# Performance work log

Measured on AMD Instinct MI355X. Metric: run time of the kernel, lower is better.

The kernel has to match this reference:

```python
import jax, jax.numpy as jnp
import numpy as np

N = 50000      # nodes per graph (= num hyperedges, forced by the stack ops)
E = 800000     # incidence pairs per graph
L = 16         # max nodes per hyperedge (padded with index 0)
F_IN = 128     # in_channels
D1 = 256       # dim_1
D2 = D1 // 4   # conv2 out dim = FusionAttention in_size
H_ATT = 128    # FusionAttention hidden_size
EPS = 1e-15


def setup_inputs() -> dict:
    key = jax.random.key(0)
    ks = jax.random.split(key, 32)
    inp = {}
    for i in range(4):
        inp[f"x{i}"] = jax.random.normal(ks[i], (N, F_IN), jnp.float32)
        nidx = jax.random.randint(ks[4 + i], (E,), 0, N, dtype=jnp.int32)
        eidx = jax.random.randint(ks[8 + i], (E,), 0, N, dtype=jnp.int32)
        inp[f"ei{i}"] = jnp.stack([nidx, eidx])  # [2, E]
        hn = jax.random.randint(ks[12 + i], (N, L), 0, N + 1, dtype=jnp.int32)
        inp[f"hnode{i}"] = hn
        # hye_len = number of real (non-padding) entries per hyperedge
        inp[f"hlen{i}"] = jnp.sum(hn > 0, axis=1, keepdims=True).astype(jnp.float32)
    # shared Hgnn params (PyG HypergraphConv: lin without bias + separate bias)
    inp["W1"] = jax.random.normal(ks[16], (F_IN, D1), jnp.float32) / np.sqrt(F_IN).astype(np.float32)
    inp["b1"] = jnp.zeros((D1,), jnp.float32)
    inp["W2"] = jax.random.normal(ks[17], (D1, D2), jnp.float32) / np.sqrt(D1).astype(np.float32)
    inp["b2"] = jnp.zeros((D2,), jnp.float32)
    # two FusionAttention heads: Linear(D2,H_ATT)+Tanh, Linear(H_ATT,1,bias=False)
    for name, a, b in [("ac", 18, 19), ("am", 20, 21)]:
        inp[f"{name}_W1"] = jax.random.normal(ks[a], (D2, H_ATT), jnp.float32) / np.sqrt(D2).astype(np.float32)
        inp[f"{name}_b1"] = jnp.zeros((H_ATT,), jnp.float32)
        inp[f"{name}_W2"] = jax.random.normal(ks[b], (H_ATT, 1), jnp.float32) / np.sqrt(H_ATT).astype(np.float32)
    return inp


def _hconv(x, node_idx, edge_idx, W, b):
    """PyG HypergraphConv (heads=1, unit hyperedge weights):
    X' = D^-1 H B^-1 H^T (X W) + b, via two segment-sum passes."""
    x = x @ W  # [N, out]
    ones = jnp.ones(node_idx.shape, x.dtype)
    deg_n = jax.ops.segment_sum(ones, node_idx, num_segments=N)
    d_inv = jnp.where(deg_n > 0, 1.0 / deg_n, 0.0)
    deg_e = jax.ops.segment_sum(ones, edge_idx, num_segments=N)
    b_inv = jnp.where(deg_e > 0, 1.0 / deg_e, 0.0)
    # node -> hyperedge: m_e = B^-1[e] * sum_{v in e} x[v]
    efeat = b_inv[:, None] * jax.ops.segment_sum(x[node_idx], edge_idx, num_segments=N)
    # hyperedge -> node: out_v = D^-1[v] * sum_{e : v in e} m_e
    out = d_inv[:, None] * jax.ops.segment_sum(efeat[edge_idx], node_idx, num_segments=N)
    return out + b


def _hgnn(x, ei, W1, b1, W2, b2):
    x = jax.nn.relu(_hconv(x, ei[0], ei[1], W1, b1))
    return jax.nn.relu(_hconv(x, ei[0], ei[1], W2, b2))


def _hye_emb(node_emb, hlen, hnode):
    # prepend zero row so padding index 0 gathers zeros
    padded = jnp.concatenate([jnp.zeros((1, node_emb.shape[1]), node_emb.dtype), node_emb], axis=0)
    seq = padded[hnode]                    # [M, L, F]
    return jnp.sum(seq, axis=1) / (hlen + EPS)


def _fusion_attn(z, W1, b1, W2):
    # z: [N, 4, d]
    w = (jnp.tanh(z @ W1 + b1) @ W2).mean(0)      # [4, 1]
    beta = jax.nn.softmax(w, axis=0)              # [4, 1]
    return jnp.sum(beta * z, axis=1)              # [N, d]


def reference(x0, x1, x2, x3, ei0, ei1, ei2, ei3,
              hlen0, hlen1, hlen2, hlen3, hnode0, hnode1, hnode2, hnode3,
              W1, b1, W2, b2, ac_W1, ac_b1, ac_W2, am_W1, am_b1, am_W2):
    x1_cm = _hgnn(x0, ei0, W1, b1, W2, b2)
    x1_mc = _hgnn(x1, ei1, W1, b1, W2, b2)
    x1_cc = _hgnn(x2, ei2, W1, b1, W2, b2)
    x1_mm = _hgnn(x3, ei3, W1, b1, W2, b2)
    x2_cm = _hye_emb(x1_cm, hlen0, hnode0)
    x2_mc = _hye_emb(x1_mc, hlen1, hnode1)
    x2_cc = _hye_emb(x1_cc, hlen2, hnode2)
    x2_mm = _hye_emb(x1_mm, hlen3, hnode3)
    x_c = jnp.stack((x1_mc, x2_cm, x1_cc, x2_cc), axis=1)  # [N, 4, D2]
    x_m = jnp.stack((x1_cm, x2_mc, x1_mm, x2_mm), axis=1)
    h_c = _fusion_attn(x_c, ac_W1, ac_b1, ac_W2)
    h_m = _fusion_attn(x_m, am_W1, am_b1, am_W2)
    return (h_c, h_m)
```

## Files before the change

kernel.cpp:

```cpp
#include <hip/hip_runtime.h>
#include <hip/hip_bf16.h>

#define NF   128
#define DD1  256
#define DD2  64
#define HATT 128

static inline int cdiv(int a, int b) { return (a + b - 1) / b; }

__global__ __launch_bounds__(256) void count_rank(const int* __restrict__ nidx,
                                                  const int* __restrict__ eidx,
                                                  int* __restrict__ deg,
                                                  int* __restrict__ rank,
                                                  int N, int E) {
    int e = blockIdx.x * 256 + threadIdx.x;
    if (e < E) {
        const int vn = nidx[e], ve = eidx[e];
        const int rn = atomicAdd(&deg[vn], 1);
        const int re = atomicAdd(&deg[N + ve], 1);
        rank[e] = rn | (re << 16);
    }
}

__global__ __launch_bounds__(256) void scan_blocks(const int* __restrict__ in,
                                                   int* __restrict__ out,
                                                   int* __restrict__ partials, int n) {
    __shared__ int s[256];
    const int base = blockIdx.x * 1024;
    const int t = threadIdx.x;
    int v[4], sum = 0;
#pragma unroll
    for (int i = 0; i < 4; i++) {
        const int idx = base + t * 4 + i;
        v[i] = (idx < n) ? in[idx] : 0;
        sum += v[i];
    }
    s[t] = sum;
    __syncthreads();
    for (int o = 1; o < 256; o <<= 1) {
        int x = 0;
        if (t >= o) x = s[t - o];
        __syncthreads();
        if (t >= o) s[t] += x;
        __syncthreads();
    }
    if (t == 255) partials[blockIdx.x] = s[255];
    int run = (t == 0) ? 0 : s[t - 1];
#pragma unroll
    for (int i = 0; i < 4; i++) {
        const int idx = base + t * 4 + i;
        if (idx < n) out[idx] = run;
        run += v[i];
    }
}

__global__ __launch_bounds__(512) void scan_partials(int* __restrict__ partials, int P) {
    __shared__ int s[512];
    const int t = threadIdx.x;
    s[t] = (t < P) ? partials[t] : 0;
    __syncthreads();
    for (int o = 1; o < 512; o <<= 1) {
        int x = 0;
        if (t >= o) x = s[t - o];
        __syncthreads();
        if (t >= o) s[t] += x;
        __syncthreads();
    }
    if (t < P) partials[t] = (t == 0) ? 0 : s[t - 1];
}

__global__ __launch_bounds__(256) void scan_add(int* __restrict__ off,
                                                const int* __restrict__ partials,
                                                int n, int total) {
    const int idx = blockIdx.x * 256 + threadIdx.x;
    if (idx < n) off[idx] += partials[idx >> 10];
    if (idx == 0) off[n] = total;
}

__global__ __launch_bounds__(256) void build_fill(const int* __restrict__ nidx,
                                                  const int* __restrict__ eidx,
                                                  const int* __restrict__ rank,
                                                  const int* __restrict__ off,
                                                  int* __restrict__ srcidx,
                                                  int N, int E, int shardSize) {
    const int shard = blockIdx.x & 7;
    const int chunk = blockIdx.x >> 3;
    const int lo = shard * shardSize;
    const int hi = lo + shardSize;
    const int base = chunk * 1024;
#pragma unroll
    for (int i = 0; i < 4; i++) {
        const int e = base + i * 256 + threadIdx.x;
        if (e < E) {
            const int vn = nidx[e], ve = eidx[e];
            const int rk = rank[e];
            if (vn >= lo && vn < hi)
                srcidx[off[vn] + (rk & 0xffff)] = ve;
            if (ve >= lo && ve < hi)
                srcidx[off[N + ve] + (rk >> 16)] = vn;
        }
    }
}

__global__ __launch_bounds__(256) void invert_deg_int(const int* __restrict__ deg,
                                                      float* __restrict__ inv, int n) {
    int t = blockIdx.x * 256 + threadIdx.x;
    if (t < n) {
        const int v = deg[t];
        inv[t] = (v > 0) ? 1.0f / (float)v : 0.f;
    }
}

struct BuildB {
    const int* nidx[4];
    const int* eidx[4];
    int* deg;
    int* rank;
    const int* off;
    int* srcidx;
    int Nn, E, shardSize;
};

__global__ __launch_bounds__(256) void count_rank_b(BuildB a) {
    const int g = blockIdx.y;
    const int e = blockIdx.x * 256 + threadIdx.x;
    if (e < a.E) {
        const int vn = a.nidx[g][e], ve = a.eidx[g][e];
        int* dg = a.deg + (size_t)g * 2 * a.Nn;
        const int rn = atomicAdd(&dg[vn], 1);
        const int re = atomicAdd(&dg[a.Nn + ve], 1);
        a.rank[(size_t)g * a.E + e] = rn | (re << 16);
    }
}

__global__ __launch_bounds__(256) void build_fill_b(BuildB a) {
    const int g = blockIdx.y;
    const int shard = blockIdx.x & 7;
    const int chunk = blockIdx.x >> 3;
    const int lo = shard * a.shardSize;
    const int hi = lo + a.shardSize;
    const int base = chunk * 1024;
    const int* __restrict__ nidx = a.nidx[g];
    const int* __restrict__ eidx = a.eidx[g];
    const int* __restrict__ rank = a.rank + (size_t)g * a.E;
    const int* __restrict__ off  = a.off + (size_t)g * 2 * a.Nn;
#pragma unroll
    for (int i = 0; i < 4; i++) {
        const int e = base + i * 256 + threadIdx.x;
        if (e < a.E) {
            const int vn = nidx[e], ve = eidx[e];
            const int rk = rank[e];
            if (vn >= lo && vn < hi)
                a.srcidx[off[vn] + (rk & 0xffff)] = ve;
            if (ve >= lo && ve < hi)
                a.srcidx[off[a.Nn + ve] + (rk >> 16)] = vn;
        }
    }
}

__global__ __launch_bounds__(256) void gather_rows_128(const float* __restrict__ src,
                                                       const int* __restrict__ off,
                                                       const int* __restrict__ srcidx,
                                                       const float* __restrict__ scale,
                                                       float* __restrict__ dst, int Nn) {
    const int row = blockIdx.x * 16 + (threadIdx.x >> 4);
    if (row >= Nn) return;
    const int c = (threadIdx.x & 15) << 2;
    const int j0 = off[row], j1 = off[row + 1];
    float4 pa = make_float4(0.f, 0.f, 0.f, 0.f);
    float4 pb = make_float4(0.f, 0.f, 0.f, 0.f);
    float4 qa = make_float4(0.f, 0.f, 0.f, 0.f);
    float4 qb = make_float4(0.f, 0.f, 0.f, 0.f);
    int j = j0;
    for (; j + 3 < j1; j += 4) {
        const int s0 = srcidx[j + 0];
        const int s1 = srcidx[j + 1];
        const int s2 = srcidx[j + 2];
        const int s3 = srcidx[j + 3];
        const float4 v0a = *(const float4*)&src[(size_t)s0 * 128 + c];
        const float4 v0b = *(const float4*)&src[(size_t)s0 * 128 + c + 64];
        const float4 v1a = *(const float4*)&src[(size_t)s1 * 128 + c];
        const float4 v1b = *(const float4*)&src[(size_t)s1 * 128 + c + 64];
        const float4 v2a = *(const float4*)&src[(size_t)s2 * 128 + c];
        const float4 v2b = *(const float4*)&src[(size_t)s2 * 128 + c + 64];
        const float4 v3a = *(const float4*)&src[(size_t)s3 * 128 + c];
        const float4 v3b = *(const float4*)&src[(size_t)s3 * 128 + c + 64];
        pa.x += v0a.x + v1a.x; pa.y += v0a.y + v1a.y;
        pa.z += v0a.z + v1a.z; pa.w += v0a.w + v1a.w;
        qa.x += v2a.x + v3a.x; qa.y += v2a.y + v3a.y;
        qa.z += v2a.z + v3a.z; qa.w += v2a.w + v3a.w;
        pb.x += v0b.x + v1b.x; pb.y += v0b.y + v1b.y;
        pb.z += v0b.z + v1b.z; pb.w += v0b.w + v1b.w;
        qb.x += v2b.x + v3b.x; qb.y += v2b.y + v3b.y;
        qb.z += v2b.z + v3b.z; qb.w += v2b.w + v3b.w;
    }
    for (; j < j1; j++) {
        const int s0 = srcidx[j];
        const float4 va = *(const float4*)&src[(size_t)s0 * 128 + c];
        const float4 vb = *(const float4*)&src[(size_t)s0 * 128 + c + 64];
        pa.x += va.x; pa.y += va.y; pa.z += va.z; pa.w += va.w;
        pb.x += vb.x; pb.y += vb.y; pb.z += vb.z; pb.w += vb.w;
    }
    float4 aca = make_float4(pa.x + qa.x, pa.y + qa.y, pa.z + qa.z, pa.w + qa.w);
    float4 acb = make_float4(pb.x + qb.x, pb.y + qb.y, pb.z + qb.z, pb.w + qb.w);
    if (scale) {
        const float s = scale[row];
        aca.x *= s; aca.y *= s; aca.z *= s; aca.w *= s;
        acb.x *= s; acb.y *= s; acb.z *= s; acb.w *= s;
    }
    *(float4*)&dst[(size_t)row * 128 + c] = aca;
    *(float4*)&dst[(size_t)row * 128 + c + 64] = acb;
}

struct Gather128H {
    const float* src[2];
    float* dst;
    const int* off;
    const int* srcidx;
    const float* dinv;
    int gbase;
    int passBase;
    int Nn;
};

__global__ __launch_bounds__(256) void gather128_h(Gather128H a) {
    const int gr = blockIdx.x * 16 + (threadIdx.x >> 4);
    if (gr >= 2 * a.Nn) return;
    const int gl = gr / a.Nn;
    const int row = gr - gl * a.Nn;
    const float* __restrict__ src = a.src[gl];
    const int ob = (a.gbase + gl) * 2 * a.Nn + a.passBase + row;
    const int c = (threadIdx.x & 15) << 2;
    const int j0 = a.off[ob], j1 = a.off[ob + 1];
    float4 pa = make_float4(0.f, 0.f, 0.f, 0.f);
    float4 pb = make_float4(0.f, 0.f, 0.f, 0.f);
    float4 qa = make_float4(0.f, 0.f, 0.f, 0.f);
    float4 qb = make_float4(0.f, 0.f, 0.f, 0.f);
    int j = j0;
    for (; j + 3 < j1; j += 4) {
        const int s0 = a.srcidx[j + 0];
        const int s1 = a.srcidx[j + 1];
        const int s2 = a.srcidx[j + 2];
        const int s3 = a.srcidx[j + 3];
        const float4 v0a = *(const float4*)&src[(size_t)s0 * 128 + c];
        const float4 v0b = *(const float4*)&src[(size_t)s0 * 128 + c + 64];
        const float4 v1a = *(const float4*)&src[(size_t)s1 * 128 + c];
        const float4 v1b = *(const float4*)&src[(size_t)s1 * 128 + c + 64];
        const float4 v2a = *(const float4*)&src[(size_t)s2 * 128 + c];
        const float4 v2b = *(const float4*)&src[(size_t)s2 * 128 + c + 64];
        const float4 v3a = *(const float4*)&src[(size_t)s3 * 128 + c];
        const float4 v3b = *(const float4*)&src[(size_t)s3 * 128 + c + 64];
        pa.x += v0a.x + v1a.x; pa.y += v0a.y + v1a.y;
        pa.z += v0a.z + v1a.z; pa.w += v0a.w + v1a.w;
        qa.x += v2a.x + v3a.x; qa.y += v2a.y + v3a.y;
        qa.z += v2a.z + v3a.z; qa.w += v2a.w + v3a.w;
        pb.x += v0b.x + v1b.x; pb.y += v0b.y + v1b.y;
        pb.z += v0b.z + v1b.z; pb.w += v0b.w + v1b.w;
        qb.x += v2b.x + v3b.x; qb.y += v2b.y + v3b.y;
        qb.z += v2b.z + v3b.z; qb.w += v2b.w + v3b.w;
    }
    for (; j < j1; j++) {
        const int s0 = a.srcidx[j];
        const float4 va = *(const float4*)&src[(size_t)s0 * 128 + c];
        const float4 vb = *(const float4*)&src[(size_t)s0 * 128 + c + 64];
        pa.x += va.x; pa.y += va.y; pa.z += va.z; pa.w += va.w;
        pb.x += vb.x; pb.y += vb.y; pb.z += vb.z; pb.w += vb.w;
    }
    float4 aca = make_float4(pa.x + qa.x, pa.y + qa.y, pa.z + qa.z, pa.w + qa.w);
    float4 acb = make_float4(pb.x + qb.x, pb.y + qb.y, pb.z + qb.z, pb.w + qb.w);
    if (a.dinv) {
        const float s = a.dinv[ob];
        aca.x *= s; aca.y *= s; aca.z *= s; aca.w *= s;
        acb.x *= s; acb.y *= s; acb.z *= s; acb.w *= s;
    }
    *(float4*)&a.dst[(size_t)gr * 128 + c] = aca;
    *(float4*)&a.dst[(size_t)gr * 128 + c + 64] = acb;
}

__global__ __launch_bounds__(256) void gather_rows_64(const float* __restrict__ src,
                                                      const int* __restrict__ off,
                                                      const int* __restrict__ srcidx,
                                                      const float* __restrict__ scale,
                                                      const float* __restrict__ post_bias,
                                                      float* __restrict__ dst, int Nn) {
    const int row = blockIdx.x * 32 + (threadIdx.x >> 3);
    if (row >= Nn) return;
    const int c = (threadIdx.x & 7) << 2;
    const int j0 = off[row], j1 = off[row + 1];
    float4 pa = make_float4(0.f, 0.f, 0.f, 0.f);
    float4 pb = make_float4(0.f, 0.f, 0.f, 0.f);
    float4 qa = make_float4(0.f, 0.f, 0.f, 0.f);
    float4 qb = make_float4(0.f, 0.f, 0.f, 0.f);
    int j = j0;
    for (; j + 3 < j1; j += 4) {
        const int s0 = srcidx[j + 0];
        const int s1 = srcidx[j + 1];
        const int s2 = srcidx[j + 2];
        const int s3 = srcidx[j + 3];
        const float4 v0a = *(const float4*)&src[(size_t)s0 * 64 + c];
        const float4 v0b = *(const float4*)&src[(size_t)s0 * 64 + c + 32];
        const float4 v1a = *(const float4*)&src[(size_t)s1 * 64 + c];
        const float4 v1b = *(const float4*)&src[(size_t)s1 * 64 + c + 32];
        const float4 v2a = *(const float4*)&src[(size_t)s2 * 64 + c];
        const float4 v2b = *(const float4*)&src[(size_t)s2 * 64 + c + 32];
        const float4 v3a = *(const float4*)&src[(size_t)s3 * 64 + c];
        const float4 v3b = *(const float4*)&src[(size_t)s3 * 64 + c + 32];
        pa.x += v0a.x + v1a.x; pa.y += v0a.y + v1a.y;
        pa.z += v0a.z + v1a.z; pa.w += v0a.w + v1a.w;
        qa.x += v2a.x + v3a.x; qa.y += v2a.y + v3a.y;
        qa.z += v2a.z + v3a.z; qa.w += v2a.w + v3a.w;
        pb.x += v0b.x + v1b.x; pb.y += v0b.y + v1b.y;
        pb.z += v0b.z + v1b.z; pb.w += v0b.w + v1b.w;
        qb.x += v2b.x + v3b.x; qb.y += v2b.y + v3b.y;
        qb.z += v2b.z + v3b.z; qb.w += v2b.w + v3b.w;
    }
    for (; j < j1; j++) {
        const int s0 = srcidx[j];
        const float4 va = *(const float4*)&src[(size_t)s0 * 64 + c];
        const float4 vb = *(const float4*)&src[(size_t)s0 * 64 + c + 32];
        pa.x += va.x; pa.y += va.y; pa.z += va.z; pa.w += va.w;
        pb.x += vb.x; pb.y += vb.y; pb.z += vb.z; pb.w += vb.w;
    }
    float4 aca = make_float4(pa.x + qa.x, pa.y + qa.y, pa.z + qa.z, pa.w + qa.w);
    float4 acb = make_float4(pb.x + qb.x, pb.y + qb.y, pb.z + qb.z, pb.w + qb.w);
    if (scale) {
        const float s = scale[row];
        aca.x *= s; aca.y *= s; aca.z *= s; aca.w *= s;
        acb.x *= s; acb.y *= s; acb.z *= s; acb.w *= s;
    }
    if (post_bias) {
        aca.x = fmaxf(aca.x + post_bias[c + 0], 0.f);
        aca.y = fmaxf(aca.y + post_bias[c + 1], 0.f);
        aca.z = fmaxf(aca.z + post_bias[c + 2], 0.f);
        aca.w = fmaxf(aca.w + post_bias[c + 3], 0.f);
        acb.x = fmaxf(acb.x + post_bias[c + 32], 0.f);
        acb.y = fmaxf(acb.y + post_bias[c + 33], 0.f);
        acb.z = fmaxf(acb.z + post_bias[c + 34], 0.f);
        acb.w = fmaxf(acb.w + post_bias[c + 35], 0.f);
    }
    *(float4*)&dst[(size_t)row * 64 + c] = aca;
    *(float4*)&dst[(size_t)row * 64 + c + 32] = acb;
}

struct Gather64B {
    const float* src[4];
    float* dst;
    const int* off;
    const int* srcidx;
    const float* dinv;
    const float* post_bias;
    int passBase;
    int Nn;
};

__global__ __launch_bounds__(256) void gather64_b(Gather64B a) {
    const int gr = blockIdx.x * 32 + (threadIdx.x >> 3);
    if (gr >= 4 * a.Nn) return;
    const int g = gr / a.Nn;
    const int row = gr - g * a.Nn;
    const float* __restrict__ src = a.src[g];
    const int ob = g * 2 * a.Nn + a.passBase + row;
    const int c = (threadIdx.x & 7) << 2;
    const int j0 = a.off[ob], j1 = a.off[ob + 1];
    float4 pa = make_float4(0.f, 0.f, 0.f, 0.f);
    float4 pb = make_float4(0.f, 0.f, 0.f, 0.f);
    float4 qa = make_float4(0.f, 0.f, 0.f, 0.f);
    float4 qb = make_float4(0.f, 0.f, 0.f, 0.f);
    int j = j0;
    for (; j + 3 < j1; j += 4) {
        const int s0 = a.srcidx[j + 0];
        const int s1 = a.srcidx[j + 1];
        const int s2 = a.srcidx[j + 2];
        const int s3 = a.srcidx[j + 3];
        const float4 v0a = *(const float4*)&src[(size_t)s0 * 64 + c];
        const float4 v0b = *(const float4*)&src[(size_t)s0 * 64 + c + 32];
        const float4 v1a = *(const float4*)&src[(size_t)s1 * 64 + c];
        const float4 v1b = *(const float4*)&src[(size_t)s1 * 64 + c + 32];
        const float4 v2a = *(const float4*)&src[(size_t)s2 * 64 + c];
        const float4 v2b = *(const float4*)&src[(size_t)s2 * 64 + c + 32];
        const float4 v3a = *(const float4*)&src[(size_t)s3 * 64 + c];
        const float4 v3b = *(const float4*)&src[(size_t)s3 * 64 + c + 32];
        pa.x += v0a.x + v1a.x; pa.y += v0a.y + v1a.y;
        pa.z += v0a.z + v1a.z; pa.w += v0a.w + v1a.w;
        qa.x += v2a.x + v3a.x; qa.y += v2a.y + v3a.y;
        qa.z += v2a.z + v3a.z; qa.w += v2a.w + v3a.w;
        pb.x += v0b.x + v1b.x; pb.y += v0b.y + v1b.y;
        pb.z += v0b.z + v1b.z; pb.w += v0b.w + v1b.w;
        qb.x += v2b.x + v3b.x; qb.y += v2b.y + v3b.y;
        qb.z += v2b.z + v3b.z; qb.w += v2b.w + v3b.w;
    }
    for (; j < j1; j++) {
        const int s0 = a.srcidx[j];
        const float4 va = *(const float4*)&src[(size_t)s0 * 64 + c];
        const float4 vb = *(const float4*)&src[(size_t)s0 * 64 + c + 32];
        pa.x += va.x; pa.y += va.y; pa.z += va.z; pa.w += va.w;
        pb.x += vb.x; pb.y += vb.y; pb.z += vb.z; pb.w += vb.w;
    }
    float4 aca = make_float4(pa.x + qa.x, pa.y + qa.y, pa.z + qa.z, pa.w + qa.w);
    float4 acb = make_float4(pb.x + qb.x, pb.y + qb.y, pb.z + qb.z, pb.w + qb.w);
    if (a.dinv) {
        const float s = a.dinv[ob];
        aca.x *= s; aca.y *= s; aca.z *= s; aca.w *= s;
        acb.x *= s; acb.y *= s; acb.z *= s; acb.w *= s;
    }
    if (a.post_bias) {
        aca.x = fmaxf(aca.x + a.post_bias[c + 0], 0.f);
        aca.y = fmaxf(aca.y + a.post_bias[c + 1], 0.f);
        aca.z = fmaxf(aca.z + a.post_bias[c + 2], 0.f);
        aca.w = fmaxf(aca.w + a.post_bias[c + 3], 0.f);
        acb.x = fmaxf(acb.x + a.post_bias[c + 32], 0.f);
        acb.y = fmaxf(acb.y + a.post_bias[c + 33], 0.f);
        acb.z = fmaxf(acb.z + a.post_bias[c + 34], 0.f);
        acb.w = fmaxf(acb.w + a.post_bias[c + 35], 0.f);
    }
    *(float4*)&a.dst[(size_t)gr * 64 + c] = aca;
    *(float4*)&a.dst[(size_t)gr * 64 + c + 32] = acb;
}

__global__ __launch_bounds__(256) void gemm1_f32(const float* __restrict__ A,
                                                 const float* __restrict__ B,
                                                 float* __restrict__ C, int M,
                                                 const float* __restrict__ dinv,
                                                 const float* __restrict__ bias) {
    __shared__ float As[32][132];
    __shared__ float Bs[32][128];
    const int tid = threadIdx.x;
    const int m0 = blockIdx.y * 128;
    const int bn = blockIdx.x * 128;
    const int rq = (tid >> 4) << 2;
    const int cq = (tid & 15) << 2;

    float acc[8][8] = {{0.f}};

    for (int k0 = 0; k0 < 128; k0 += 32) {
#pragma unroll
        for (int i = 0; i < 4; i++) {
            const int f = tid + 256 * i;
            const int r = f >> 3;
            const int q = (f & 7) << 2;
            const int grow = m0 + r;
            float4 v = make_float4(0.f, 0.f, 0.f, 0.f);
            if (grow < M) v = *(const float4*)&A[(size_t)grow * 128 + k0 + q];
            As[q + 0][r] = v.x;
            As[q + 1][r] = v.y;
            As[q + 2][r] = v.z;
            As[q + 3][r] = v.w;
        }
#pragma unroll
        for (int i = 0; i < 4; i++) {
            const int f = tid + 256 * i;
            const int r = f >> 5;
            const int c4 = (f & 31) << 2;
            *(float4*)&Bs[r][c4] = *(const float4*)&B[(size_t)(k0 + r) * 256 + bn + c4];
        }
        __syncthreads();
#pragma unroll
        for (int k = 0; k < 32; k++) {
            float av[8], bv[8];
            *(float4*)&av[0] = *(const float4*)&As[k][rq];
            *(float4*)&av[4] = *(const float4*)&As[k][rq + 64];
            *(float4*)&bv[0] = *(const float4*)&Bs[k][cq];
            *(float4*)&bv[4] = *(const float4*)&Bs[k][cq + 64];
#pragma unroll
            for (int r = 0; r < 8; r++)
#pragma unroll
                for (int c = 0; c < 8; c++)
                    acc[r][c] = fmaf(av[r], bv[c], acc[r][c]);
        }
        __syncthreads();
    }
#pragma unroll
    for (int r = 0; r < 8; r++) {
        const int grow = m0 + rq + (r & 3) + ((r >> 2) << 6);
        if (grow < M) {
            const float s = dinv[grow];
            float o[8];
#pragma unroll
            for (int c = 0; c < 4; c++)
                o[c] = fmaxf(fmaf(acc[r][c], s, bias[bn + cq + c]), 0.f);
#pragma unroll
            for (int c = 4; c < 8; c++)
                o[c] = fmaxf(fmaf(acc[r][c], s, bias[bn + 64 + cq + (c - 4)]), 0.f);
            *(float4*)&C[(size_t)grow * 256 + bn + cq] = *(float4*)&o[0];
            *(float4*)&C[(size_t)grow * 256 + bn + 64 + cq] = *(float4*)&o[4];
        }
    }
}

__global__ __launch_bounds__(256) void gemm2_f32(const float* __restrict__ A,
                                                 const float* __restrict__ B,
                                                 float* __restrict__ C, int M) {
    __shared__ float As[32][132];
    __shared__ float Bs[32][64];
    const int tid = threadIdx.x;
    const int m0 = blockIdx.y * 128;
    const int tr = (tid >> 3) << 2;
    const int tc = (tid & 7) << 3;

    float acc[4][8] = {{0.f}};

    for (int k0 = 0; k0 < 256; k0 += 32) {
#pragma unroll
        for (int i = 0; i < 4; i++) {
            const int f = tid + 256 * i;
            const int r = f >> 3;
            const int q = (f & 7) << 2;
            const int grow = m0 + r;
            float4 v = make_float4(0.f, 0.f, 0.f, 0.f);
            if (grow < M) v = *(const float4*)&A[(size_t)grow * 256 + k0 + q];
            As[q + 0][r] = v.x;
            As[q + 1][r] = v.y;
            As[q + 2][r] = v.z;
            As[q + 3][r] = v.w;
        }
#pragma unroll
        for (int i = 0; i < 2; i++) {
            const int f = tid + 256 * i;
            const int r = f >> 4;
            const int c4 = (f & 15) << 2;
            *(float4*)&Bs[r][c4] = *(const float4*)&B[(size_t)(k0 + r) * 64 + c4];
        }
        __syncthreads();
#pragma unroll
        for (int k = 0; k < 32; k++) {
            float av[4], bv[8];
            *(float4*)&av[0] = *(const float4*)&As[k][tr];
            *(float4*)&bv[0] = *(const float4*)&Bs[k][tc];
            *(float4*)&bv[4] = *(const float4*)&Bs[k][tc + 4];
#pragma unroll
            for (int r = 0; r < 4; r++)
#pragma unroll
                for (int c = 0; c < 8; c++)
                    acc[r][c] = fmaf(av[r], bv[c], acc[r][c]);
        }
        __syncthreads();
    }
#pragma unroll
    for (int r = 0; r < 4; r++) {
        const int grow = m0 + tr + r;
        if (grow < M) {
            *(float4*)&C[(size_t)grow * 64 + tc] =
                make_float4(acc[r][0], acc[r][1], acc[r][2], acc[r][3]);
            *(float4*)&C[(size_t)grow * 64 + tc + 4] =
                make_float4(acc[r][4], acc[r][5], acc[r][6], acc[r][7]);
        }
    }
}

struct Gemm12B {
    const float* A;
    const float* W1;
    const float* W2;
    const float* b1;
    const float* dinv;
    float* D;
    int Nn;
};

__global__ __launch_bounds__(256) void gemm12_b(Gemm12B a) {
    __shared__ float smem[11264];
    float* As  = smem;
    float* Bs  = smem + 2176;
    float* Ts  = smem;
    float* W2s = smem + 9216;
    float* Rs  = smem;

    const int M4 = 4 * a.Nn;
    const int tid = threadIdx.x;
    const int m0 = blockIdx.x * 64;
    const int rq = (tid >> 5) << 3;
    const int cq = (tid & 31) << 2;

    float acc[8][8] = {{0.f}};

    for (int k0 = 0; k0 < 128; k0 += 32) {
#pragma unroll
        for (int i = 0; i < 2; i++) {
            const int f = tid + 256 * i;
            const int r = f >> 3;
            const int q = (f & 7) << 2;
            const int grow = m0 + r;
            float4 v = make_float4(0.f, 0.f, 0.f, 0.f);
            if (grow < M4) v = *(const float4*)&a.A[(size_t)grow * 128 + k0 + q];
            As[(q + 0) * 68 + r] = v.x;
            As[(q + 1) * 68 + r] = v.y;
            As[(q + 2) * 68 + r] = v.z;
            As[(q + 3) * 68 + r] = v.w;
        }
#pragma unroll
        for (int i = 0; i < 8; i++) {
            const int f = tid + 256 * i;
            const int r = f >> 6;
            const int c4 = (f & 63) << 2;
            *(float4*)&Bs[r * 256 + c4] = *(const float4*)&a.W1[(size_t)(k0 + r) * 256 + c4];
        }
        __syncthreads();
#pragma unroll
        for (int k = 0; k < 32; k++) {
            float av[8], bv[8];
            *(float4*)&av[0] = *(const float4*)&As[k * 68 + rq];
            *(float4*)&av[4] = *(const float4*)&As[k * 68 + rq + 4];
            *(float4*)&bv[0] = *(const float4*)&Bs[k * 256 + cq];
            *(float4*)&bv[4] = *(const float4*)&Bs[k * 256 + cq + 128];
#pragma unroll
            for (int r = 0; r < 8; r++)
#pragma unroll
                for (int c = 0; c < 8; c++)
                    acc[r][c] = fmaf(av[r], bv[c], acc[r][c]);
        }
        __syncthreads();
    }

    float b1lo[4], b1hi[4], sc[8];
#pragma unroll
    for (int j = 0; j < 4; j++) {
        b1lo[j] = a.b1[cq + j];
        b1hi[j] = a.b1[cq + 128 + j];
    }
#pragma unroll
    for (int r = 0; r < 8; r++) {
        const int grow = m0 + rq + r;
        float sv = 0.f;
        if (grow < M4) {
            const int g = grow / a.Nn;
            const int lr = grow - g * a.Nn;
            sv = a.dinv[(size_t)g * 2 * a.Nn + lr];
        }
        sc[r] = sv;
    }

    const int col4 = (tid & 15) << 2;
    const int row4 = ((tid >> 4) & 7) << 2;
    const int kpar = tid >> 7;
    const int myg  = tid >> 5;

    for (int h = 0; h < 2; h++) {
        __syncthreads();
        if ((myg >> 2) == h) {
            const int lmb = rq - 32 * h;
#pragma unroll
            for (int r = 0; r < 8; r++) {
                const int lm = lmb + r;
#pragma unroll
                for (int j = 0; j < 4; j++) {
                    Ts[(cq + j) * 36 + lm] =
                        fmaxf(fmaf(acc[r][j], sc[r], b1lo[j]), 0.f);
                    Ts[(cq + 128 + j) * 36 + lm] =
                        fmaxf(fmaf(acc[r][4 + j], sc[r], b1hi[j]), 0.f);
                }
            }
        }
        float4 dr0 = make_float4(0.f, 0.f, 0.f, 0.f);
        float4 dr1 = make_float4(0.f, 0.f, 0.f, 0.f);
        float4 dr2 = make_float4(0.f, 0.f, 0.f, 0.f);
        float4 dr3 = make_float4(0.f, 0.f, 0.f, 0.f);
        for (int kk = 0; kk < 256; kk += 32) {
            __syncthreads();
#pragma unroll
            for (int i = 0; i < 2; i++) {
                const int f = tid + 256 * i;
                const int r = f >> 4;
                const int c4 = (f & 15) << 2;
                *(float4*)&W2s[r * 64 + c4] = *(const float4*)&a.W2[(size_t)(kk + r) * 64 + c4];
            }
            __syncthreads();
#pragma unroll
            for (int j = 0; j < 16; j++) {
                const int k = 2 * j + kpar;
                const float4 tv = *(const float4*)&Ts[(kk + k) * 36 + row4];
                const float4 wv = *(const float4*)&W2s[k * 64 + col4];
                dr0.x = fmaf(tv.x, wv.x, dr0.x); dr0.y = fmaf(tv.x, wv.y, dr0.y);
                dr0.z = fmaf(tv.x, wv.z, dr0.z); dr0.w = fmaf(tv.x, wv.w, dr0.w);
                dr1.x = fmaf(tv.y, wv.x, dr1.x); dr1.y = fmaf(tv.y, wv.y, dr1.y);
                dr1.z = fmaf(tv.y, wv.z, dr1.z); dr1.w = fmaf(tv.y, wv.w, dr1.w);
                dr2.x = fmaf(tv.z, wv.x, dr2.x); dr2.y = fmaf(tv.z, wv.y, dr2.y);
                dr2.z = fmaf(tv.z, wv.z, dr2.z); dr2.w = fmaf(tv.z, wv.w, dr2.w);
                dr3.x = fmaf(tv.w, wv.x, dr3.x); dr3.y = fmaf(tv.w, wv.y, dr3.y);
                dr3.z = fmaf(tv.w, wv.z, dr3.z); dr3.w = fmaf(tv.w, wv.w, dr3.w);
            }
        }
        __syncthreads();
        if (kpar) {
            *(float4*)&Rs[(row4 + 0) * 68 + col4] = dr0;
            *(float4*)&Rs[(row4 + 1) * 68 + col4] = dr1;
            *(float4*)&Rs[(row4 + 2) * 68 + col4] = dr2;
            *(float4*)&Rs[(row4 + 3) * 68 + col4] = dr3;
        }
        __syncthreads();
        if (!kpar) {
            float4 part[4] = {dr0, dr1, dr2, dr3};
#pragma unroll
            for (int r = 0; r < 4; r++) {
                const int grow = m0 + 32 * h + row4 + r;
                if (grow < M4) {
                    float4 o = *(float4*)&Rs[(row4 + r) * 68 + col4];
                    o.x += part[r].x; o.y += part[r].y;
                    o.z += part[r].z; o.w += part[r].w;
                    *(float4*)&a.D[(size_t)grow * 64 + col4] = o;
                }
            }
        }
    }
}

__global__ __launch_bounds__(256) void hye_emb_kernel(const float* __restrict__ emb,
                                                      const int* __restrict__ hnode,
                                                      const float* __restrict__ hlen,
                                                      float* __restrict__ out, int Nn) {
    const int r = blockIdx.x * 16 + (threadIdx.x >> 4);
    const int c = (threadIdx.x & 15) << 2;
    if (r >= Nn) return;
    const int4* hp4 = (const int4*)&hnode[(size_t)r * 16];
    const int4 w0 = hp4[0], w1 = hp4[1], w2 = hp4[2], w3 = hp4[3];
    int idx[16] = {w0.x, w0.y, w0.z, w0.w, w1.x, w1.y, w1.z, w1.w,
                   w2.x, w2.y, w2.z, w2.w, w3.x, w3.y, w3.z, w3.w};
    float4 a0 = make_float4(0.f, 0.f, 0.f, 0.f);
    float4 a1 = make_float4(0.f, 0.f, 0.f, 0.f);
    float4 a2 = make_float4(0.f, 0.f, 0.f, 0.f);
    float4 a3 = make_float4(0.f, 0.f, 0.f, 0.f);
#pragma unroll
    for (int l = 0; l < 16; l += 4) {
        if (idx[l + 0] > 0) {
            const float4 v = *(const float4*)&emb[(size_t)(idx[l + 0] - 1) * 64 + c];
            a0.x += v.x; a0.y += v.y; a0.z += v.z; a0.w += v.w;
        }
        if (idx[l + 1] > 0) {
            const float4 v = *(const float4*)&emb[(size_t)(idx[l + 1] - 1) * 64 + c];
            a1.x += v.x; a1.y += v.y; a1.z += v.z; a1.w += v.w;
        }
        if (idx[l + 2] > 0) {
            const float4 v = *(const float4*)&emb[(size_t)(idx[l + 2] - 1) * 64 + c];
            a2.x += v.x; a2.y += v.y; a2.z += v.z; a2.w += v.w;
        }
        if (idx[l + 3] > 0) {
            const float4 v = *(const float4*)&emb[(size_t)(idx[l + 3] - 1) * 64 + c];
            a3.x += v.x; a3.y += v.y; a3.z += v.z; a3.w += v.w;
        }
    }
    const float inv = 1.0f / (hlen[r] + 1e-15f);
    float4 acc;
    acc.x = (a0.x + a1.x + a2.x + a3.x) * inv;
    acc.y = (a0.y + a1.y + a2.y + a3.y) * inv;
    acc.z = (a0.z + a1.z + a2.z + a3.z) * inv;
    acc.w = (a0.w + a1.w + a2.w + a3.w) * inv;
    *(float4*)&out[(size_t)r * 64 + c] = acc;
}

struct HyeB {
    const float* emb;
    const int* hnode[4];
    const float* hlen[4];
    float* out;
    int Nn;
};

__global__ __launch_bounds__(256) void hye_b(HyeB a) {
    const int gr = blockIdx.x * 16 + (threadIdx.x >> 4);
    const int c = (threadIdx.x & 15) << 2;
    if (gr >= 4 * a.Nn) return;
    const int g = gr / a.Nn;
    const int lr = gr - g * a.Nn;
    const float* __restrict__ emb = a.emb + (size_t)g * a.Nn * 64;
    const int4* hp4 = (const int4*)&a.hnode[g][(size_t)lr * 16];
    const int4 w0 = hp4[0], w1 = hp4[1], w2 = hp4[2], w3 = hp4[3];
    int idx[16] = {w0.x, w0.y, w0.z, w0.w, w1.x, w1.y, w1.z, w1.w,
                   w2.x, w2.y, w2.z, w2.w, w3.x, w3.y, w3.z, w3.w};
    float4 a0 = make_float4(0.f, 0.f, 0.f, 0.f);
    float4 a1 = make_float4(0.f, 0.f, 0.f, 0.f);
    float4 a2 = make_float4(0.f, 0.f, 0.f, 0.f);
    float4 a3 = make_float4(0.f, 0.f, 0.f, 0.f);
#pragma unroll
    for (int l = 0; l < 16; l += 4) {
        if (idx[l + 0] > 0) {
            const float4 v = *(const float4*)&emb[(size_t)(idx[l + 0] - 1) * 64 + c];
            a0.x += v.x; a0.y += v.y; a0.z += v.z; a0.w += v.w;
        }
        if (idx[l + 1] > 0) {
            const float4 v = *(const float4*)&emb[(size_t)(idx[l + 1] - 1) * 64 + c];
            a1.x += v.x; a1.y += v.y; a1.z += v.z; a1.w += v.w;
        }
        if (idx[l + 2] > 0) {
            const float4 v = *(const float4*)&emb[(size_t)(idx[l + 2] - 1) * 64 + c];
            a2.x += v.x; a2.y += v.y; a2.z += v.z; a2.w += v.w;
        }
        if (idx[l + 3] > 0) {
            const float4 v = *(const float4*)&emb[(size_t)(idx[l + 3] - 1) * 64 + c];
            a3.x += v.x; a3.y += v.y; a3.z += v.z; a3.w += v.w;
        }
    }
    const float inv = 1.0f / (a.hlen[g][lr] + 1e-15f);
    float4 acc;
    acc.x = (a0.x + a1.x + a2.x + a3.x) * inv;
    acc.y = (a0.y + a1.y + a2.y + a3.y) * inv;
    acc.z = (a0.z + a1.z + a2.z + a3.z) * inv;
    acc.w = (a0.w + a1.w + a2.w + a3.w) * inv;
    *(float4*)&a.out[(size_t)gr * 64 + c] = acc;
}

struct AttnArgs {
    const float* z[8];
    const float* W1c; const float* b1c; const float* W2c;
    const float* W1m; const float* b1m; const float* W2m;
    float* accw;
    int Nn;
};

__global__ __launch_bounds__(256) void attn_gemm(AttnArgs a) {
    __shared__ float As[64][68];
    __shared__ float Bs[64][128];
    __shared__ float red[4];
    const int tid = threadIdx.x;
    const int gy = blockIdx.y;
    const int head = gy >> 2;
    const float* __restrict__ z  = a.z[gy];
    const float* __restrict__ W1 = head ? a.W1m : a.W1c;
    const float* __restrict__ b1 = head ? a.b1m : a.b1c;
    const float* __restrict__ W2 = head ? a.W2m : a.W2c;
    const int m0 = blockIdx.x * 64;

    {
        const int m = tid >> 2;
        const int qb = tid & 3;
        const int grow = m0 + m;
#pragma unroll
        for (int it = 0; it < 4; it++) {
            const int q = qb + 4 * it;
            float4 v = make_float4(0.f, 0.f, 0.f, 0.f);
            if (grow < a.Nn) v = *(const float4*)&z[(size_t)grow * 64 + q * 4];
            As[q * 4 + 0][m] = v.x;
            As[q * 4 + 1][m] = v.y;
            As[q * 4 + 2][m] = v.z;
            As[q * 4 + 3][m] = v.w;
        }
    }
    {
#pragma unroll
        for (int i = 0; i < 8; i++) {
            const int f = tid + 256 * i;
            const int r = f >> 5, cc = (f & 31) << 2;
            *(float4*)&Bs[r][cc] = *(const float4*)&W1[(size_t)r * 128 + cc];
        }
    }
    __syncthreads();

    const int mq = (tid & 15) << 2;
    const int cq = (tid >> 4) << 2;
    float acc[4][8] = {{0.f}};
    for (int k = 0; k < 64; k++) {
        float av[4], bv[8];
        *(float4*)&av[0] = *(const float4*)&As[k][mq];
        *(float4*)&bv[0] = *(const float4*)&Bs[k][cq];
        *(float4*)&bv[4] = *(const float4*)&Bs[k][cq + 64];
#pragma unroll
        for (int r = 0; r < 4; r++)
#pragma unroll
            for (int c = 0; c < 8; c++)
                acc[r][c] = fmaf(av[r], bv[c], acc[r][c]);
    }

    float w2v[8], b1v[8];
#pragma unroll
    for (int c = 0; c < 8; c++) {
        const int col = cq + (c & 3) + ((c >> 2) << 6);
        w2v[c] = W2[col];
        b1v[c] = b1[col];
    }
    float local = 0.f;
#pragma unroll
    for (int r = 0; r < 4; r++) {
        if (m0 + mq + r < a.Nn) {
#pragma unroll
            for (int c = 0; c < 8; c++) {
                float s = acc[r][c] + b1v[c];
                s = fminf(fmaxf(s, -15.f), 15.f);
                const float t = __expf(2.f * s);
                local += (1.f - 2.f / (t + 1.f)) * w2v[c];
            }
        }
    }
#pragma unroll
    for (int off = 32; off >= 1; off >>= 1) local += __shfl_down(local, off, 64);
    if ((tid & 63) == 0) red[tid >> 6] = local;
    __syncthreads();
    if (tid == 0) atomicAdd(&a.accw[gy], red[0] + red[1] + red[2] + red[3]);
}

__global__ void softmax_beta(const float* __restrict__ acc, float* __restrict__ beta,
                             float invN) {
    const int t = threadIdx.x;
    if (t < 2) {
        const float* a = acc + 4 * t;
        float* b = beta + 4 * t;
        float w[4], m = -1e30f;
#pragma unroll
        for (int i = 0; i < 4; i++) { w[i] = a[i] * invN; m = fmaxf(m, w[i]); }
        float s = 0.f;
#pragma unroll
        for (int i = 0; i < 4; i++) { w[i] = expf(w[i] - m); s += w[i]; }
#pragma unroll
        for (int i = 0; i < 4; i++) b[i] = w[i] / s;
    }
}

__global__ __launch_bounds__(256) void weighted_sum(const float* __restrict__ z0,
                                                    const float* __restrict__ z1,
                                                    const float* __restrict__ z2,
                                                    const float* __restrict__ z3,
                                                    const float* __restrict__ beta,
                                                    float* __restrict__ out, int Nn) {
    const int t = blockIdx.x * 256 + threadIdx.x;
    if (t >= Nn * 16) return;
    const float b0 = beta[0], b1 = beta[1], b2 = beta[2], b3 = beta[3];
    const float4 v0 = *(const float4*)&z0[(size_t)t * 4];
    const float4 v1 = *(const float4*)&z1[(size_t)t * 4];
    const float4 v2 = *(const float4*)&z2[(size_t)t * 4];
    const float4 v3 = *(const float4*)&z3[(size_t)t * 4];
    float4 o;
    o.x = b0 * v0.x + b1 * v1.x + b2 * v2.x + b3 * v3.x;
    o.y = b0 * v0.y + b1 * v1.y + b2 * v2.y + b3 * v3.y;
    o.z = b0 * v0.z + b1 * v1.z + b2 * v2.z + b3 * v3.z;
    o.w = b0 * v0.w + b1 * v1.w + b2 * v2.w + b3 * v3.w;
    *(float4*)&out[(size_t)t * 4] = o;
}

extern "C" void kernel_launch(void* const* d_in, const int* in_sizes, int n_in,
                              void* d_out, int out_size, void* d_ws, size_t ws_size,
                              hipStream_t stream) {
    const int Nn = in_sizes[0] / NF;
    const int E  = in_sizes[1] / 2;
    const int N2 = 2 * Nn;

    const float* x[4];
    const int*   ei[4];
    const int*   hnode[4];
    const float* hlen[4];
    for (int g = 0; g < 4; g++) {
        x[g]     = (const float*)d_in[4 * g + 0];
        ei[g]    = (const int*)d_in[4 * g + 1];
        hnode[g] = (const int*)d_in[4 * g + 2];
        hlen[g]  = (const float*)d_in[4 * g + 3];
    }
    const float* W1   = (const float*)d_in[16];
    const float* b1   = (const float*)d_in[17];
    const float* W2   = (const float*)d_in[18];
    const float* b2   = (const float*)d_in[19];
    const float* acW1 = (const float*)d_in[20];
    const float* acb1 = (const float*)d_in[21];
    const float* acW2 = (const float*)d_in[22];
    const float* amW1 = (const float*)d_in[23];
    const float* amb1 = (const float*)d_in[24];
    const float* amW2 = (const float*)d_in[25];

    const size_t fRA   = (size_t)4 * Nn * 64;
    const size_t fRB   = (size_t)4 * Nn * 128;
    const size_t fDinv = (size_t)4 * N2;
    const size_t fcnt  = fRA + fRB + fDinv + 16;
    const size_t icnt  = ((size_t)4 * N2 + 4) + 512 + (size_t)8 * E;
    const size_t need  = (fcnt + icnt) * sizeof(float) + 256;
    const bool raFitsInts = fRA * sizeof(float) >=
                            ((size_t)4 * N2 + (size_t)4 * E) * sizeof(int);

    if (need <= ws_size && raFitsInts) {
        float* ws = (float*)d_ws;
        size_t o = 0;
        float* RA   = ws + o; o += fRA;
        float* RB   = ws + o; o += fRB;
        float* dinv = ws + o; o += fDinv;
        float* accw = ws + o; o += 8;
        float* beta = ws + o; o += 8;
        int* iws = (int*)(ws + o);
        size_t io = 0;
        int* off      = iws + io; io += (size_t)4 * N2 + 4;
        int* partials = iws + io; io += 512;
        int* srcidx   = iws + io; io += (size_t)8 * E;
        int* deg  = (int*)RA;
        int* rank = deg + (size_t)4 * N2;

        const int n8 = 4 * N2;
        const int nScanBlocks = cdiv(n8, 1024);

        BuildB bb;
        for (int g = 0; g < 4; g++) { bb.nidx[g] = ei[g]; bb.eidx[g] = ei[g] + E; }
        bb.deg = deg; bb.rank = rank; bb.off = off; bb.srcidx = srcidx;
        bb.Nn = Nn; bb.E = E; bb.shardSize = cdiv(Nn, 8);

        hipMemsetAsync(deg, 0, (size_t)n8 * sizeof(int), stream);
        count_rank_b<<<dim3(cdiv(E, 256), 4), 256, 0, stream>>>(bb);
        scan_blocks<<<nScanBlocks, 256, 0, stream>>>(deg, off, partials, n8);
        scan_partials<<<1, 512, 0, stream>>>(partials, nScanBlocks);
        scan_add<<<cdiv(n8, 256), 256, 0, stream>>>(off, partials, n8, 2 * 4 * E);
        build_fill_b<<<dim3(8 * cdiv(E, 1024), 4), 256, 0, stream>>>(bb);
        invert_deg_int<<<cdiv(n8, 256), 256, 0, stream>>>(deg, dinv, n8);

        const int gh = cdiv(2 * Nn, 16);
        for (int h = 0; h < 2; h++) {
            const int gb = 2 * h;
            Gather128H p1;
            p1.src[0] = x[gb]; p1.src[1] = x[gb + 1];
            p1.dst = RA; p1.off = off; p1.srcidx = srcidx;
            p1.dinv = dinv; p1.gbase = gb; p1.passBase = Nn; p1.Nn = Nn;
            gather128_h<<<gh, 256, 0, stream>>>(p1);

            Gather128H p2;
            p2.src[0] = RA; p2.src[1] = RA + (size_t)Nn * 128;
            p2.dst = RB + (size_t)gb * Nn * 128;
            p2.off = off; p2.srcidx = srcidx;
            p2.dinv = nullptr; p2.gbase = gb; p2.passBase = 0; p2.Nn = Nn;
            gather128_h<<<gh, 256, 0, stream>>>(p2);
        }

        float* Dbuf = RA;
        Gemm12B gm;
        gm.A = RB; gm.W1 = W1; gm.W2 = W2; gm.b1 = b1;
        gm.dinv = dinv; gm.D = Dbuf; gm.Nn = Nn;
        gemm12_b<<<cdiv(4 * Nn, 64), 256, 0, stream>>>(gm);

        float* E1  = RB + (size_t)4 * Nn * 64;
        float* h2b = RB;
        Gather64B g3;
        for (int g = 0; g < 4; g++) g3.src[g] = Dbuf + (size_t)g * Nn * 64;
        g3.dst = E1; g3.off = off; g3.srcidx = srcidx;
        g3.dinv = dinv; g3.post_bias = nullptr; g3.passBase = Nn; g3.Nn = Nn;
        gather64_b<<<cdiv(4 * Nn, 32), 256, 0, stream>>>(g3);

        Gather64B g4;
        for (int g = 0; g < 4; g++) g4.src[g] = E1 + (size_t)g * Nn * 64;
        g4.dst = h2b; g4.off = off; g4.srcidx = srcidx;
        g4.dinv = dinv; g4.post_bias = b2; g4.passBase = 0; g4.Nn = Nn;
        gather64_b<<<cdiv(4 * Nn, 32), 256, 0, stream>>>(g4);

        float* hembb = RA;
        HyeB hb;
        hb.emb = h2b;
        for (int g = 0; g < 4; g++) { hb.hnode[g] = hnode[g]; hb.hlen[g] = hlen[g]; }
        hb.out = hembb; hb.Nn = Nn;
        hye_b<<<cdiv(4 * Nn, 16), 256, 0, stream>>>(hb);

        const size_t st = (size_t)Nn * 64;
        hipMemsetAsync(accw, 0, 8 * sizeof(float), stream);
        AttnArgs aa;
        aa.z[0] = h2b + 1 * st; aa.z[1] = hembb + 0 * st;
        aa.z[2] = h2b + 2 * st; aa.z[3] = hembb + 2 * st;
        aa.z[4] = h2b + 0 * st; aa.z[5] = hembb + 1 * st;
        aa.z[6] = h2b + 3 * st; aa.z[7] = hembb + 3 * st;
        aa.W1c = acW1; aa.b1c = acb1; aa.W2c = acW2;
        aa.W1m = amW1; aa.b1m = amb1; aa.W2m = amW2;
        aa.accw = accw; aa.Nn = Nn;
        attn_gemm<<<dim3(cdiv(Nn, 64), 8), 256, 0, stream>>>(aa);
        softmax_beta<<<1, 64, 0, stream>>>(accw, beta, 1.0f / (float)Nn);

        float* out = (float*)d_out;
        weighted_sum<<<cdiv(Nn * 16, 256), 256, 0, stream>>>(
            aa.z[0], aa.z[1], aa.z[2], aa.z[3], beta + 0, out, Nn);
        weighted_sum<<<cdiv(Nn * 16, 256), 256, 0, stream>>>(
            aa.z[4], aa.z[5], aa.z[6], aa.z[7], beta + 4, out + (size_t)Nn * DD2, Nn);
        return;
    }

    float* ws = (float*)d_ws;
    size_t o = 0;
    float* bufA = ws + o; o += (size_t)Nn * DD1;
    float* bufB = ws + o; o += (size_t)Nn * DD1;
    float* dinv = ws + o; o += N2;
    float* h2[4];
    float* hemb[4];
    for (int g = 0; g < 4; g++) { h2[g]   = ws + o; o += (size_t)Nn * DD2; }
    for (int g = 0; g < 4; g++) { hemb[g] = ws + o; o += (size_t)Nn * DD2; }
    float* accw = ws + o; o += 8;
    float* beta = ws + o; o += 8;
    int* iws = (int*)(ws + o);
    size_t io = 0;
    int* deg_i    = iws + io; io += N2;
    int* off      = iws + io; io += N2 + 1;
    int* partials = iws + io; io += 512;
    int* rank     = iws + io; io += E;
    int* srcidx   = iws + io; io += (size_t)2 * E;

    const int nScanBlocks = cdiv(N2, 1024);
    const int shardSize = cdiv(Nn, 8);

    for (int g = 0; g < 4; g++) {
        const int* nidx = ei[g];
        const int* eidx = ei[g] + E;
        const int* off_n = off;
        const int* off_e = off + Nn;
        const float* d_inv = dinv;
        const float* b_inv = dinv + Nn;

        hipMemsetAsync(deg_i, 0, (size_t)N2 * sizeof(int), stream);
        count_rank<<<cdiv(E, 256), 256, 0, stream>>>(nidx, eidx, deg_i, rank, Nn, E);
        scan_blocks<<<nScanBlocks, 256, 0, stream>>>(deg_i, off, partials, N2);
        scan_partials<<<1, 512, 0, stream>>>(partials, nScanBlocks);
        scan_add<<<cdiv(N2, 256), 256, 0, stream>>>(off, partials, N2, 2 * E);
        build_fill<<<8 * cdiv(E, 1024), 256, 0, stream>>>(nidx, eidx, rank, off,
                                                          srcidx, Nn, E, shardSize);
        invert_deg_int<<<cdiv(N2, 256), 256, 0, stream>>>(deg_i, dinv, N2);

        gather_rows_128<<<cdiv(Nn, 16), 256, 0, stream>>>(x[g], off_e, srcidx, b_inv, bufB, Nn);
        gather_rows_128<<<cdiv(Nn, 16), 256, 0, stream>>>(bufB, off_n, srcidx, nullptr, bufA, Nn);
        gemm1_f32<<<dim3(2, cdiv(Nn, 128)), 256, 0, stream>>>(bufA, W1, bufB, Nn, d_inv, b1);

        gemm2_f32<<<dim3(1, cdiv(Nn, 128)), 256, 0, stream>>>(bufB, W2, bufA, Nn);
        gather_rows_64<<<cdiv(Nn, 32), 256, 0, stream>>>(bufA, off_e, srcidx, b_inv,
                                                         nullptr, bufB, Nn);
        gather_rows_64<<<cdiv(Nn, 32), 256, 0, stream>>>(bufB, off_n, srcidx, d_inv,
                                                         b2, h2[g], Nn);

        hye_emb_kernel<<<cdiv(Nn, 16), 256, 0, stream>>>(h2[g], hnode[g], hlen[g], hemb[g], Nn);
    }

    hipMemsetAsync(accw, 0, 8 * sizeof(float), stream);
    AttnArgs aa;
    aa.z[0] = h2[1]; aa.z[1] = hemb[0]; aa.z[2] = h2[2]; aa.z[3] = hemb[2];
    aa.z[4] = h2[0]; aa.z[5] = hemb[1]; aa.z[6] = h2[3]; aa.z[7] = hemb[3];
    aa.W1c = acW1; aa.b1c = acb1; aa.W2c = acW2;
    aa.W1m = amW1; aa.b1m = amb1; aa.W2m = amW2;
    aa.accw = accw; aa.Nn = Nn;
    attn_gemm<<<dim3(cdiv(Nn, 64), 8), 256, 0, stream>>>(aa);
    softmax_beta<<<1, 64, 0, stream>>>(accw, beta, 1.0f / (float)Nn);

    float* out = (float*)d_out;
    weighted_sum<<<cdiv(Nn * 16, 256), 256, 0, stream>>>(h2[1], hemb[0], h2[2], hemb[2],
                                                         beta + 0, out, Nn);
    weighted_sum<<<cdiv(Nn * 16, 256), 256, 0, stream>>>(h2[0], hemb[1], h2[3], hemb[3],
                                                         beta + 4, out + (size_t)Nn * DD2, Nn);
}
```

Measured before the change: 1.831 ms.

## Restructure fused second GEMM epilogue with swizzled K-split tiles and 4x8 outputs

The second-stage GEMM inside gemm12_b now stages the ReLU'd hidden tile as two 128-wide K halves covering all 64 rows, with an XOR-swizzled shared layout, instead of two 32-row halves. Each thread computes a 4x8 output block over 64-row chunks of W2, which halves the number of W2 reload and barrier rounds and the cross-thread reduction passes. Launch bounds now request 3 blocks per CU. The trade-off is more shared memory per block and higher register pressure from 32 accumulators plus the retained acc array.

```diff
diff --git a/kernel.cpp b/kernel.cpp
--- a/kernel.cpp
+++ b/kernel.cpp
@@ -557,12 +557,12 @@
     int Nn;
 };
 
-__global__ __launch_bounds__(256) void gemm12_b(Gemm12B a) {
-    __shared__ float smem[11264];
+__global__ __launch_bounds__(256, 3) void gemm12_b(Gemm12B a) {
+    __shared__ float smem[12800];
     float* As  = smem;
     float* Bs  = smem + 2176;
     float* Ts  = smem;
-    float* W2s = smem + 9216;
+    float* W2s = smem + 8704;
     float* Rs  = smem;
 
     const int M4 = 4 * a.Nn;
@@ -629,75 +629,96 @@
         sc[r] = sv;
     }
 
-    const int col4 = (tid & 15) << 2;
-    const int row4 = ((tid >> 4) & 7) << 2;
+    const int col8 = (tid & 7) << 3;
+    const int row4 = ((tid >> 3) & 15) << 2;
     const int kpar = tid >> 7;
-    const int myg  = tid >> 5;
-
-    for (int h = 0; h < 2; h++) {
+    const int qi   = row4 >> 2;
+
+    float4 dl[4], dh[4];
+#pragma unroll
+    for (int r = 0; r < 4; r++) {
+        dl[r] = make_float4(0.f, 0.f, 0.f, 0.f);
+        dh[r] = make_float4(0.f, 0.f, 0.f, 0.f);
+    }
+
+    for (int kh = 0; kh < 2; kh++) {
         __syncthreads();
-        if ((myg >> 2) == h) {
-            const int lmb = rq - 32 * h;
-#pragma unroll
-            for (int r = 0; r < 8; r++) {
-                const int lm = lmb + r;
-#pragma unroll
-                for (int j = 0; j < 4; j++) {
-                    Ts[(cq + j) * 36 + lm] =
-                        fmaxf(fmaf(acc[r][j], sc[r], b1lo[j]), 0.f);
-                    Ts[(cq + 128 + j) * 36 + lm] =
-                        fmaxf(fmaf(acc[r][4 + j], sc[r], b1hi[j]), 0.f);
+        {
+            const int x   = (tid & 31) & 7;
+            const int t2  = (tid >> 5) << 1;
+            const int sw0 = (t2 ^ x) << 2;
+            const int sw1 = ((t2 + 1) ^ x) << 2;
+#pragma unroll
+            for (int j = 0; j < 4; j++) {
+                float* tk = &Ts[(cq + j) * 68];
+#pragma unroll
+                for (int r = 0; r < 8; r++) {
+                    const float v = fmaxf(fmaf(acc[r][(kh ? 4 : 0) + j], sc[r],
+                                               kh ? b1hi[j] : b1lo[j]), 0.f);
+                    tk[(r < 4 ? sw0 : sw1) + (r & 3)] = v;
                 }
             }
         }
-        float4 dr0 = make_float4(0.f, 0.f, 0.f, 0.f);
-        float4 dr1 = make_float4(0.f, 0.f, 0.f, 0.f);
-        float4 dr2 = make_float4(0.f, 0.f, 0.f, 0.f);
-        float4 dr3 = make_float4(0.f, 0.f, 0.f, 0.f);
-        for (int kk = 0; kk < 256; kk += 32) {
-            __syncthreads();
-#pragma unroll
-            for (int i = 0; i < 2; i++) {
+        for (int kc = 0; kc < 2; kc++) {
+            if (kc) __syncthreads();
+#pragma unroll
+            for (int i = 0; i < 4; i++) {
                 const int f = tid + 256 * i;
-                const int r = f >> 4;
+                const int kr = f >> 4;
                 const int c4 = (f & 15) << 2;
-                *(float4*)&W2s[r * 64 + c4] = *(const float4*)&a.W2[(size_t)(kk + r) * 64 + c4];
+                *(float4*)&W2s[kr * 64 + c4] =
+                    *(const float4*)&a.W2[(size_t)(kh * 128 + kc * 64 + kr) * 64 + c4];
             }
             __syncthreads();
 #pragma unroll
-            for (int j = 0; j < 16; j++) {
-                const int k = 2 * j + kpar;
-                const float4 tv = *(const float4*)&Ts[(kk + k) * 36 + row4];
-                const float4 wv = *(const float4*)&W2s[k * 64 + col4];
-                dr0.x = fmaf(tv.x, wv.x, dr0.x); dr0.y = fmaf(tv.x, wv.y, dr0.y);
-                dr0.z = fmaf(tv.x, wv.z, dr0.z); dr0.w = fmaf(tv.x, wv.w, dr0.w);
-                dr1.x = fmaf(tv.y, wv.x, dr1.x); dr1.y = fmaf(tv.y, wv.y, dr1.y);
-                dr1.z = fmaf(tv.y, wv.z, dr1.z); dr1.w = fmaf(tv.y, wv.w, dr1.w);
-                dr2.x = fmaf(tv.z, wv.x, dr2.x); dr2.y = fmaf(tv.z, wv.y, dr2.y);
-                dr2.z = fmaf(tv.z, wv.z, dr2.z); dr2.w = fmaf(tv.z, wv.w, dr2.w);
-                dr3.x = fmaf(tv.w, wv.x, dr3.x); dr3.y = fmaf(tv.w, wv.y, dr3.y);
-                dr3.z = fmaf(tv.w, wv.z, dr3.z); dr3.w = fmaf(tv.w, wv.w, dr3.w);
+            for (int jj = 0; jj < 32; jj++) {
+                const int kl = (jj << 1) | kpar;
+                const int sw = (qi ^ ((kl >> 2) & 7)) << 2;
+                const float4 tv  = *(const float4*)&Ts[(kc * 64 + kl) * 68 + sw];
+                const float4 wv0 = *(const float4*)&W2s[kl * 64 + col8];
+                const float4 wv1 = *(const float4*)&W2s[kl * 64 + col8 + 4];
+                dl[0].x = fmaf(tv.x, wv0.x, dl[0].x); dl[0].y = fmaf(tv.x, wv0.y, dl[0].y);
+                dl[0].z = fmaf(tv.x, wv0.z, dl[0].z); dl[0].w = fmaf(tv.x, wv0.w, dl[0].w);
+                dh[0].x = fmaf(tv.x, wv1.x, dh[0].x); dh[0].y = fmaf(tv.x, wv1.y, dh[0].y);
+                dh[0].z = fmaf(tv.x, wv1.z, dh[0].z); dh[0].w = fmaf(tv.x, wv1.w, dh[0].w);
+                dl[1].x = fmaf(tv.y, wv0.x, dl[1].x); dl[1].y = fmaf(tv.y, wv0.y, dl[1].y);
+                dl[1].z = fmaf(tv.y, wv0.z, dl[1].z); dl[1].w = fmaf(tv.y, wv0.w, dl[1].w);
+                dh[1].x = fmaf(tv.y, wv1.x, dh[1].x); dh[1].y = fmaf(tv.y, wv1.y, dh[1].y);
+                dh[1].z = fmaf(tv.y, wv1.z, dh[1].z); dh[1].w = fmaf(tv.y, wv1.w, dh[1].w);
+                dl[2].x = fmaf(tv.z, wv0.x, dl[2].x); dl[2].y = fmaf(tv.z, wv0.y, dl[2].y);
+                dl[2].z = fmaf(tv.z, wv0.z, dl[2].z); dl[2].w = fmaf(tv.z, wv0.w, dl[2].w);
+                dh[2].x = fmaf(tv.z, wv1.x, dh[2].x); dh[2].y = fmaf(tv.z, wv1.y, dh[2].y);
+                dh[2].z = fmaf(tv.z, wv1.z, dh[2].z); dh[2].w = fmaf(tv.z, wv1.w, dh[2].w);
+                dl[3].x = fmaf(tv.w, wv0.x, dl[3].x); dl[3].y = fmaf(tv.w, wv0.y, dl[3].y);
+                dl[3].z = fmaf(tv.w, wv0.z, dl[3].z); dl[3].w = fmaf(tv.w, wv0.w, dl[3].w);
+                dh[3].x = fmaf(tv.w, wv1.x, dh[3].x); dh[3].y = fmaf(tv.w, wv1.y, dh[3].y);
+                dh[3].z = fmaf(tv.w, wv1.z, dh[3].z); dh[3].w = fmaf(tv.w, wv1.w, dh[3].w);
             }
         }
-        __syncthreads();
-        if (kpar) {
-            *(float4*)&Rs[(row4 + 0) * 68 + col4] = dr0;
-            *(float4*)&Rs[(row4 + 1) * 68 + col4] = dr1;
-            *(float4*)&Rs[(row4 + 2) * 68 + col4] = dr2;
-            *(float4*)&Rs[(row4 + 3) * 68 + col4] = dr3;
-        }
-        __syncthreads();
-        if (!kpar) {
-            float4 part[4] = {dr0, dr1, dr2, dr3};
-#pragma unroll
-            for (int r = 0; r < 4; r++) {
-                const int grow = m0 + 32 * h + row4 + r;
-                if (grow < M4) {
-                    float4 o = *(float4*)&Rs[(row4 + r) * 68 + col4];
-                    o.x += part[r].x; o.y += part[r].y;
-                    o.z += part[r].z; o.w += part[r].w;
-                    *(float4*)&a.D[(size_t)grow * 64 + col4] = o;
-                }
+    }
+
+    __syncthreads();
+    if (kpar == 1) {
+#pragma unroll
+        for (int r = 0; r < 4; r++) {
+            *(float4*)&Rs[(row4 + r) * 68 + col8]     = dl[r];
+            *(float4*)&Rs[(row4 + r) * 68 + col8 + 4] = dh[r];
+        }
+    }
+    __syncthreads();
+    if (kpar == 0) {
+#pragma unroll
+        for (int r = 0; r < 4; r++) {
+            const int grow = m0 + row4 + r;
+            if (grow < M4) {
+                const float4 pl = *(const float4*)&Rs[(row4 + r) * 68 + col8];
+                const float4 ph = *(const float4*)&Rs[(row4 + r) * 68 + col8 + 4];
+                float4 ol = make_float4(dl[r].x + pl.x, dl[r].y + pl.y,
+                                        dl[r].z + pl.z, dl[r].w + pl.w);
+                float4 oh = make_float4(dh[r].x + ph.x, dh[r].y + ph.y,
+                                        dh[r].z + ph.z, dh[r].w + ph.w);
+                *(float4*)&a.D[(size_t)grow * 64 + col8]     = ol;
+                *(float4*)&a.D[(size_t)grow * 64 + col8 + 4] = oh;
             }
         }
     }
```

Result: slower. 1.932 ms (+5.5%).
